# Kernel tuning notes

Measured on AMD Instinct MI355X. Metric: run time of the kernel, lower is better.

## Reference

```python
import jax, jax.numpy as jnp
import numpy as np

T_ITERS = 10
EPS = 1e-5


def setup_inputs() -> dict:
    key = jax.random.key(0)
    B, C, H, W = 64, 256, 56, 56
    X = jax.random.normal(key, (B, C, H, W), dtype=jnp.float32)
    # running_rot buffer: orthogonal rotation per group (g=1)
    M = np.random.default_rng(0).standard_normal((C, C)).astype(np.float32)
    q, _ = np.linalg.qr(M)
    running_rot = jnp.asarray(q[None, :, :])  # [g=1, d, d]
    return {"X": X, "running_rot": running_rot}


def _whiten(X, g, nc):
    # X: [B, C, H, W] -> x: [g, d, m] with m = B*H*W (training-mode IterNorm)
    B, C, H, W = X.shape
    x = jnp.transpose(X, (1, 0, 2, 3)).reshape(g, nc, -1)
    m = x.shape[-1]
    mean = jnp.mean(x, axis=-1, keepdims=True)          # [g, d, 1]
    xc = x - mean                                        # [g, d, m]
    I = jnp.broadcast_to(jnp.eye(nc, dtype=X.dtype), (g, nc, nc))
    Sigma = EPS * I + jnp.matmul(xc, jnp.swapaxes(xc, 1, 2)) * (1.0 / m)
    # rTr = 1 / trace(Sigma) per group
    rTr = 1.0 / jnp.sum(Sigma * I, axis=(1, 2), keepdims=True)  # [g,1,1]
    Sigma_N = Sigma * rTr
    # Newton-Schulz iteration: P_{k+1} = 1.5 P_k - 0.5 P_k^3 Sigma_N
    P = I
    for _ in range(T_ITERS):
        P3 = jnp.matmul(jnp.matmul(P, P), P)
        P = 1.5 * P - 0.5 * jnp.matmul(P3, Sigma_N)
    wm = P * jnp.sqrt(rTr)                               # whitening matrix [g,d,d]
    xn = jnp.matmul(wm, xc)                              # [g, d, m]
    return xn.reshape(C, B, H, W).transpose(1, 0, 2, 3)  # back to [B,C,H,W]


def reference(X, running_rot):
    g, _, nc = running_rot.shape
    B, C, H, W = X.shape
    X_hat = _whiten(X, g, nc)                            # [B, C, H, W]
    Xg = X_hat.reshape(B, g, nc, H, W)
    # rotate whitened features: Q^T alignment, einsum('bgchw,gdc->bgdhw')
    Xr = jnp.einsum('bgchw,gdc->bgdhw', Xg, running_rot)
    return Xr.reshape(B, C, H, W)
```

## Files before the change

### kernel.cpp

```cpp
#include <hip/hip_runtime.h>
#include <math.h>

#define HWn   3136
#define Cn    256
#define KCPB  49
#define NCHUNK 3136
#define INV_M (1.0f/200704.0f)
#define EPSc  1e-5f

typedef __attribute__((ext_vector_type(4))) float f32x4;
typedef __attribute__((ext_vector_type(8))) short s16x8;
typedef __attribute__((ext_vector_type(4))) unsigned short u16x4;

static __device__ __forceinline__ unsigned short f2bf(float f) {
  unsigned int u = __builtin_bit_cast(unsigned int, f);
  u = (u + 0x7fffu + ((u >> 16) & 1u)) >> 16;
  return (unsigned short)u;
}

__global__ __launch_bounds__(1024) void k_gram(const float* __restrict__ X,
                                               float* __restrict__ Gp,
                                               float* __restrict__ Sp,
                                               int nparts) {
  __shared__ __align__(16) unsigned short lds[2][256 * 64];
  const int t = threadIdx.x, p = blockIdx.x;
  const int w = t >> 6, l = t & 63, a = l & 15, g = l >> 4;
  const int swzA = (a & 7) << 3;
  const int crow = t >> 4, sg = t & 15;

  f32x4 acc[16];
#pragma unroll
  for (int j = 0; j < 16; ++j) acc[j] = (f32x4){0.f, 0.f, 0.f, 0.f};
  float sum4[4] = {0.f, 0.f, 0.f, 0.f};
  float vx[16];

  const int start = (int)(((long)NCHUNK * p) / nparts);
  const int end   = (int)(((long)NCHUNK * (p + 1)) / nparts);

#define G_LOADS(CH)                                                           \
  {                                                                           \
    const int b_ = (CH) / KCPB, kc_ = (CH) % KCPB;                            \
    const float* xb_ = X + (long)b_ * Cn * HWn + kc_ * 64;                    \
    _Pragma("unroll")                                                         \
    for (int p4 = 0; p4 < 4; ++p4) {                                          \
      const float4 v = *(const float4*)(xb_ + (long)(p4 * 64 + crow) * HWn + sg * 4); \
      vx[p4 * 4 + 0] = v.x; vx[p4 * 4 + 1] = v.y;                             \
      vx[p4 * 4 + 2] = v.z; vx[p4 * 4 + 3] = v.w;                             \
    }                                                                         \
  }

#define G_CVTWR(BUF)                                                          \
  {                                                                           \
    _Pragma("unroll")                                                         \
    for (int p4 = 0; p4 < 4; ++p4) {                                          \
      const int c_ = p4 * 64 + crow;                                          \
      sum4[p4] += (vx[p4 * 4 + 0] + vx[p4 * 4 + 1])                           \
                + (vx[p4 * 4 + 2] + vx[p4 * 4 + 3]);                          \
      u16x4 h;                                                                \
      h.x = f2bf(vx[p4 * 4 + 0]); h.y = f2bf(vx[p4 * 4 + 1]);                 \
      h.z = f2bf(vx[p4 * 4 + 2]); h.w = f2bf(vx[p4 * 4 + 3]);                 \
      *(u16x4*)(&lds[BUF][0] + ((c_ * 64 + sg * 4) ^ ((c_ & 7) << 3))) = h;   \
    }                                                                         \
  }

  G_LOADS(start);
  G_CVTWR(0);
  __syncthreads();

  for (int ch = start; ch < end; ++ch) {
    const int cur = (ch - start) & 1;
    if (ch + 1 < end) G_LOADS(ch + 1);
    const unsigned short* tile = &lds[cur][0];
#pragma unroll
    for (int kk = 0; kk < 64; kk += 32) {
      const s16x8 fw = *(const s16x8*)(tile + (((w * 16 + a) * 64 + kk + g * 8) ^ swzA));
#pragma unroll
      for (int j = 0; j < 16; ++j) {
        const s16x8 fj = *(const s16x8*)(tile + (((j * 16 + a) * 64 + kk + g * 8) ^ swzA));
        acc[j] = __builtin_amdgcn_mfma_f32_16x16x32_bf16(fw, fj, acc[j], 0, 0, 0);
      }
    }
    if (ch + 1 < end) G_CVTWR(cur ^ 1);
    __syncthreads();
  }
#undef G_LOADS
#undef G_CVTWR

  float* gout = Gp + (long)p * 65536;
#pragma unroll
  for (int j = 0; j < 16; ++j)
#pragma unroll
    for (int r = 0; r < 4; ++r)
      gout[(16 * w + 4 * g + r) * 256 + 16 * j + a] = acc[j][r];

#pragma unroll
  for (int p4 = 0; p4 < 4; ++p4) {
    float s = sum4[p4];
    s += __shfl_xor(s, 1);
    s += __shfl_xor(s, 2);
    s += __shfl_xor(s, 4);
    s += __shfl_xor(s, 8);
    if (a == 0) Sp[(long)p * 256 + p4 * 64 + w * 4 + g] = s;
  }
}

__global__ __launch_bounds__(1024) void k_reduce(const float* __restrict__ Gp,
                                                 const float* __restrict__ Sp,
                                                 float* __restrict__ Sigma,
                                                 float* __restrict__ P0,
                                                 float* __restrict__ diag,
                                                 float* __restrict__ meansum,
                                                 int nparts) {
  __shared__ float red[4][256];
  __shared__ float msh[256];
  const int t = threadIdx.x, c = t & 255, g = t >> 8, j = blockIdx.x;
  const long e = (long)j * 256 + c;
  const int p0 = (nparts * g) >> 2, p1 = (nparts * (g + 1)) >> 2;

  {
    float s = 0.f;
    for (int p = p0; p < p1; ++p) s += Sp[(long)p * 256 + c];
    red[g][c] = s;
  }
  __syncthreads();
  if (g == 0) msh[c] = (red[0][c] + red[1][c]) + (red[2][c] + red[3][c]);
  __syncthreads();

  {
    const float* gp = Gp + (long)p0 * 65536 + e;
    const int np = p1 - p0;
    float s0 = 0.f, s1 = 0.f, s2 = 0.f, s3 = 0.f;
    int p = 0;
#pragma unroll 2
    for (; p + 4 <= np; p += 4) {
      s0 += gp[(long)(p + 0) * 65536];
      s1 += gp[(long)(p + 1) * 65536];
      s2 += gp[(long)(p + 2) * 65536];
      s3 += gp[(long)(p + 3) * 65536];
    }
    for (; p < np; ++p) s0 += gp[(long)p * 65536];
    red[g][c] = (s0 + s1) + (s2 + s3);
  }
  __syncthreads();

  if (g == 0) {
    const float tot = (red[0][c] + red[1][c]) + (red[2][c] + red[3][c]);
    const float mc = msh[c] * INV_M;
    const float mj = msh[j] * INV_M;
    const float sig = tot * INV_M - mj * mc + ((j == c) ? EPSc : 0.f);
    Sigma[e] = sig;
    if (c == j) diag[j] = sig;
    if (j == 0) meansum[c] = msh[c];
  } else if (g == 1) {
    P0[e] = (j == c) ? 1.f : 0.f;
  }
}

__global__ void k_prep(const float* __restrict__ diag, float* __restrict__ scal) {
  __shared__ float r[256];
  const int c = threadIdx.x;
  r[c] = diag[c];
  __syncthreads();
  for (int st = 128; st > 0; st >>= 1) {
    if (c < st) r[c] += r[c + st];
    __syncthreads();
  }
  if (c == 0) {
    const float tr = r[0];
    scal[0] = tr;
    scal[1] = 1.0f / tr;
    scal[2] = sqrtf(1.0f / tr);
  }
}

__global__ __launch_bounds__(1024) void k_ns(const float* __restrict__ Ps,
                                             float* __restrict__ Pd,
                                             const float* __restrict__ Sig,
                                             const float* __restrict__ scal) {
  __shared__ __align__(16) float PT[256][4];
  __shared__ __align__(16) float red[4][256][4];
  const int t = threadIdx.x, c = t & 255, kh = t >> 8, k0 = kh * 64;
  const int r0 = blockIdx.x * 4;

  PT[c][kh] = Ps[(r0 + kh) * 256 + c];
  __syncthreads();

  f32x4 acc;

#define NS_PHASE(BPTR)                                                        \
  {                                                                           \
    acc = (f32x4){0.f, 0.f, 0.f, 0.f};                                        \
    const float* Bb = (BPTR) + (long)k0 * 256 + c;                            \
    _Pragma("unroll 8")                                                       \
    for (int kk = 0; kk < 64; ++kk) {                                         \
      const float b = Bb[(long)kk * 256];                                     \
      const f32x4 a4 = *(const f32x4*)&PT[k0 + kk][0];                        \
      acc += a4 * b;                                                          \
    }                                                                         \
    *(f32x4*)&red[kh][c][0] = acc;                                            \
    __syncthreads();                                                          \
  }

#define NS_COMBINE()                                                          \
  {                                                                           \
    const f32x4 vs = (*(const f32x4*)&red[0][c][0] + *(const f32x4*)&red[1][c][0]) \
                   + (*(const f32x4*)&red[2][c][0] + *(const f32x4*)&red[3][c][0]); \
    if (kh == 0) *(f32x4*)&PT[c][0] = vs;                                     \
    __syncthreads();                                                          \
  }

  NS_PHASE(Ps);
  NS_COMBINE();
  NS_PHASE(Ps);
  NS_COMBINE();
  NS_PHASE(Sig);

  const float rTr = scal[1];
  const float t3 = ((red[0][c][kh] + red[1][c][kh]) + (red[2][c][kh] + red[3][c][kh]));
  const float pr = Ps[(r0 + kh) * 256 + c];
  Pd[(r0 + kh) * 256 + c] = 1.5f * pr - 0.5f * rTr * t3;
#undef NS_PHASE
#undef NS_COMBINE
}

__global__ void k_makeA(const float* __restrict__ rot, const float* __restrict__ P,
                        const float* __restrict__ scal, const float* __restrict__ meansum,
                        unsigned short* __restrict__ Abf, float* __restrict__ bias) {
  __shared__ float Rw[8][256];
  __shared__ float Tw[8][256];
  const int r0 = blockIdx.x * 8, c = threadIdx.x;
#pragma unroll
  for (int r = 0; r < 8; ++r) Rw[r][c] = rot[(r0 + r) * 256 + c];
  __syncthreads();
  float t[8];
#pragma unroll
  for (int r = 0; r < 8; ++r) t[r] = 0.f;
  for (int k = 0; k < 256; ++k) {
    const float pv = P[k * 256 + c];
#pragma unroll
    for (int r = 0; r < 8; ++r) t[r] += Rw[r][k] * pv;
  }
  const float s = scal[2];
  const float mc = meansum[c] * INV_M;
#pragma unroll
  for (int r = 0; r < 8; ++r) {
    const float av = t[r] * s;
    Abf[(r0 + r) * 256 + c] = f2bf(av);
    Tw[r][c] = av * mc;
  }
  __syncthreads();
  for (int st = 128; st > 0; st >>= 1) {
    if (c < st) {
#pragma unroll
      for (int r = 0; r < 8; ++r) Tw[r][c] += Tw[r][c + st];
    }
    __syncthreads();
  }
  if (c == 0) {
#pragma unroll
    for (int r = 0; r < 8; ++r) bias[r0 + r] = Tw[r][0];
  }
}

__global__ __launch_bounds__(1024) void k_apply(const float* __restrict__ X,
                                                const unsigned short* __restrict__ Abf,
                                                const float* __restrict__ bias,
                                                float* __restrict__ out) {
  __shared__ __align__(16) unsigned short lds[2][64 * 256];
  const int t = threadIdx.x, w = t >> 6, l = t & 63, a = l & 15, g = l >> 4;
  const int bid = blockIdx.x;
  const int b = bid >> 3, strip = bid & 7;
  const int ch0 = (49 * strip) >> 3, ch1 = (49 * (strip + 1)) >> 3;

  const int d = 16 * w + a;
  s16x8 af[8];
#pragma unroll
  for (int kk8 = 0; kk8 < 8; ++kk8)
    af[kk8] = *(const s16x8*)(Abf + d * 256 + kk8 * 32 + g * 8);
  const float bd = bias[d];

  const float* xbase = X + (long)b * Cn * HWn;
  float* obase = out + (long)b * Cn * HWn;
  float vx[16];

#define A_LOADS(CH)                                                           \
  {                                                                           \
    const int s0_ = (CH) * 64;                                                \
    _Pragma("unroll")                                                         \
    for (int p4 = 0; p4 < 4; ++p4) {                                          \
      const int c4_ = p4 * 16 + w;                                            \
      const float* xp_ = xbase + (long)(c4_ * 4) * HWn + s0_ + l;             \
      vx[p4 * 4 + 0] = xp_[0];                                                \
      vx[p4 * 4 + 1] = xp_[HWn];                                              \
      vx[p4 * 4 + 2] = xp_[2 * HWn];                                          \
      vx[p4 * 4 + 3] = xp_[3 * HWn];                                          \
    }                                                                         \
  }

#define A_CVTWR(BUF)                                                          \
  {                                                                           \
    _Pragma("unroll")                                                         \
    for (int p4 = 0; p4 < 4; ++p4) {                                          \
      const int c4_ = p4 * 16 + w;                                            \
      u16x4 h;                                                                \
      h.x = f2bf(vx[p4 * 4 + 0]); h.y = f2bf(vx[p4 * 4 + 1]);                 \
      h.z = f2bf(vx[p4 * 4 + 2]); h.w = f2bf(vx[p4 * 4 + 3]);                 \
      *(u16x4*)(&lds[BUF][0] + ((l * 256 + c4_ * 4) ^ ((l & 7) << 3))) = h;   \
    }                                                                         \
  }

  A_LOADS(ch0);
  A_CVTWR(0);
  __syncthreads();

  for (int ch = ch0; ch < ch1; ++ch) {
    const int cur = (ch - ch0) & 1;
    if (ch + 1 < ch1) A_LOADS(ch + 1);

    const unsigned short* tile = &lds[cur][0];
    f32x4 acc[4];
#pragma unroll
    for (int st = 0; st < 4; ++st) acc[st] = (f32x4){0.f, 0.f, 0.f, 0.f};
#pragma unroll
    for (int kk8 = 0; kk8 < 8; ++kk8) {
#pragma unroll
      for (int st = 0; st < 4; ++st) {
        const s16x8 xf = *(const s16x8*)(tile + (((st * 16 + a) * 256 + kk8 * 32 + g * 8) ^ ((a & 7) << 3)));
        acc[st] = __builtin_amdgcn_mfma_f32_16x16x32_bf16(xf, af[kk8], acc[st], 0, 0, 0);
      }
    }
    const int s0 = ch * 64;
#pragma unroll
    for (int st = 0; st < 4; ++st) {
      const f32x4 o = acc[st] - bd;
      *(f32x4*)(obase + (long)d * HWn + s0 + st * 16 + 4 * g) = o;
    }

    if (ch + 1 < ch1) A_CVTWR(cur ^ 1);
    __syncthreads();
  }
#undef A_LOADS
#undef A_CVTWR
}

extern "C" void kernel_launch(void* const* d_in, const int* in_sizes, int n_in,
                              void* d_out, int out_size, void* d_ws, size_t ws_size,
                              hipStream_t stream) {
  const float* X = (const float*)d_in[0];
  const float* rot = (const float*)d_in[1];
  float* out = (float*)d_out;

  auto need = [](int np) -> size_t {
    return (size_t)4 * ((size_t)np * 65536 + (size_t)np * 256 + 3 * 65536
                        + 256 + 256 + 16 + 256)
         + (size_t)2 * 65536;
  };
  int nparts = 256;
  while (nparts > 4 && need(nparts) > ws_size) nparts >>= 1;

  float* w = (float*)d_ws;
  float* Gp = w;       w += (size_t)nparts * 65536;
  float* Sp = w;       w += (size_t)nparts * 256;
  float* Sigma = w;    w += 65536;
  float* P0 = w;       w += 65536;
  float* P1 = w;       w += 65536;
  float* diag = w;     w += 256;
  float* meansum = w;  w += 256;
  float* scal = w;     w += 16;
  float* bias = w;     w += 256;
  unsigned short* Abf = (unsigned short*)w;

  k_gram<<<dim3(nparts), dim3(1024), 0, stream>>>(X, Gp, Sp, nparts);
  k_reduce<<<dim3(256), dim3(1024), 0, stream>>>(Gp, Sp, Sigma, P0, diag, meansum, nparts);
  k_prep<<<dim3(1), dim3(256), 0, stream>>>(diag, scal);
  float* ps = P0;
  float* pd = P1;
  for (int i = 0; i < 10; ++i) {
    k_ns<<<dim3(64), dim3(1024), 0, stream>>>(ps, pd, Sigma, scal);
    float* tmp = ps; ps = pd; pd = tmp;
  }
  k_makeA<<<dim3(32), dim3(256), 0, stream>>>(rot, ps, scal, meansum, Abf, bias);
  k_apply<<<dim3(512), dim3(1024), 0, stream>>>(X, Abf, bias, out);
}
```

Measured before the change: 312.9 us.

## Fuse Newton-Schulz iterations and makeA into one persistent kernel with grid barrier

Replaces the prep kernel, ten separate Newton-Schulz launches and the makeA kernel with a single persistent 64-block kernel. It computes the trace locally, peels the first iteration analytically (P1 = 1.5I - 0.5 rTr Sigma), and synchronises blocks between iterations with an atomic spin barrier. The intent is to remove about eleven kernel launch gaps from this serial chain. It also vectorises the Gram partial reduction with float4 loads across 16 slices and uses nontemporal stores for the output. The spin barrier relies on all 64 blocks being co-resident, and the barrier counter is reset in the preceding kernel.

```diff
diff --git a/kernel.cpp b/kernel.cpp
--- a/kernel.cpp
+++ b/kernel.cpp
@@ -16,6 +16,18 @@
   unsigned int u = __builtin_bit_cast(unsigned int, f);
   u = (u + 0x7fffu + ((u >> 16) & 1u)) >> 16;
   return (unsigned short)u;
+}
+
+static __device__ __forceinline__ void grid_sync(unsigned int* bar, unsigned int target) {
+  __syncthreads();
+  if (threadIdx.x == 0) {
+    __threadfence();
+    atomicAdd(bar, 1u);
+    while (__hip_atomic_load(bar, __ATOMIC_RELAXED, __HIP_MEMORY_SCOPE_AGENT) < target)
+      __builtin_amdgcn_s_sleep(2);
+  }
+  __syncthreads();
+  __threadfence();
 }
 
 __global__ __launch_bounds__(1024) void k_gram(const float* __restrict__ X,
@@ -107,83 +119,83 @@
 __global__ __launch_bounds__(1024) void k_reduce(const float* __restrict__ Gp,
                                                  const float* __restrict__ Sp,
                                                  float* __restrict__ Sigma,
-                                                 float* __restrict__ P0,
                                                  float* __restrict__ diag,
                                                  float* __restrict__ meansum,
+                                                 unsigned int* __restrict__ bar,
                                                  int nparts) {
-  __shared__ float red[4][256];
+  __shared__ float redA[4][256];
   __shared__ float msh[256];
-  const int t = threadIdx.x, c = t & 255, g = t >> 8, j = blockIdx.x;
-  const long e = (long)j * 256 + c;
-  const int p0 = (nparts * g) >> 2, p1 = (nparts * (g + 1)) >> 2;
+  __shared__ __align__(16) float redB[16][256];
+  const int t = threadIdx.x, j = blockIdx.x;
+  const int c = t & 255, g = t >> 8;
 
   {
     float s = 0.f;
-    for (int p = p0; p < p1; ++p) s += Sp[(long)p * 256 + c];
-    red[g][c] = s;
-  }
-  __syncthreads();
-  if (g == 0) msh[c] = (red[0][c] + red[1][c]) + (red[2][c] + red[3][c]);
-  __syncthreads();
+    const int pa0 = (nparts * g) >> 2, pa1 = (nparts * (g + 1)) >> 2;
+    for (int p = pa0; p < pa1; ++p) s += Sp[(long)p * 256 + c];
+    redA[g][c] = s;
+  }
+  __syncthreads();
+  if (g == 0) msh[c] = (redA[0][c] + redA[1][c]) + (redA[2][c] + redA[3][c]);
 
   {
-    const float* gp = Gp + (long)p0 * 65536 + e;
-    const int np = p1 - p0;
-    float s0 = 0.f, s1 = 0.f, s2 = 0.f, s3 = 0.f;
-    int p = 0;
-#pragma unroll 2
-    for (; p + 4 <= np; p += 4) {
-      s0 += gp[(long)(p + 0) * 65536];
-      s1 += gp[(long)(p + 1) * 65536];
-      s2 += gp[(long)(p + 2) * 65536];
-      s3 += gp[(long)(p + 3) * 65536];
-    }
-    for (; p < np; ++p) s0 += gp[(long)p * 65536];
-    red[g][c] = (s0 + s1) + (s2 + s3);
-  }
-  __syncthreads();
-
-  if (g == 0) {
-    const float tot = (red[0][c] + red[1][c]) + (red[2][c] + red[3][c]);
-    const float mc = msh[c] * INV_M;
+    const int c4 = (t & 63) * 4, sl = t >> 6;
+    const int pb0 = (nparts * sl) >> 4, pb1 = (nparts * (sl + 1)) >> 4;
+    const float* gp = Gp + (long)pb0 * 65536 + (long)j * 256 + c4;
+    f32x4 s4 = (f32x4){0.f, 0.f, 0.f, 0.f};
+    for (int p = pb0; p < pb1; ++p) { s4 += *(const f32x4*)gp; gp += 65536; }
+    *(f32x4*)&redB[sl][c4] = s4;
+  }
+  __syncthreads();
+
+  if (t < 256) {
+    float t0 = 0.f, t1 = 0.f;
+#pragma unroll
+    for (int sl = 0; sl < 16; sl += 2) { t0 += redB[sl][t]; t1 += redB[sl + 1][t]; }
+    const float tot = t0 + t1;
+    const float mc = msh[t] * INV_M;
     const float mj = msh[j] * INV_M;
-    const float sig = tot * INV_M - mj * mc + ((j == c) ? EPSc : 0.f);
-    Sigma[e] = sig;
-    if (c == j) diag[j] = sig;
-    if (j == 0) meansum[c] = msh[c];
-  } else if (g == 1) {
-    P0[e] = (j == c) ? 1.f : 0.f;
-  }
-}
-
-__global__ void k_prep(const float* __restrict__ diag, float* __restrict__ scal) {
-  __shared__ float r[256];
-  const int c = threadIdx.x;
-  r[c] = diag[c];
-  __syncthreads();
-  for (int st = 128; st > 0; st >>= 1) {
-    if (c < st) r[c] += r[c + st];
-    __syncthreads();
-  }
-  if (c == 0) {
-    const float tr = r[0];
-    scal[0] = tr;
-    scal[1] = 1.0f / tr;
-    scal[2] = sqrtf(1.0f / tr);
-  }
-}
-
-__global__ __launch_bounds__(1024) void k_ns(const float* __restrict__ Ps,
-                                             float* __restrict__ Pd,
-                                             const float* __restrict__ Sig,
-                                             const float* __restrict__ scal) {
+    const float sig = tot * INV_M - mj * mc + ((j == t) ? EPSc : 0.f);
+    Sigma[(long)j * 256 + t] = sig;
+    if (t == j) diag[j] = sig;
+    if (j == 0) {
+      meansum[t] = msh[t];
+      if (t == 0)
+        __hip_atomic_store(bar, 0u, __ATOMIC_RELAXED, __HIP_MEMORY_SCOPE_SYSTEM);
+    }
+  }
+}
+
+__global__ __launch_bounds__(1024) void k_ns_fused(const float* __restrict__ Sig,
+                                                   float* __restrict__ P0,
+                                                   float* __restrict__ P1,
+                                                   const float* __restrict__ diag,
+                                                   const float* __restrict__ rot,
+                                                   const float* __restrict__ meansum,
+                                                   unsigned int* __restrict__ bar,
+                                                   unsigned short* __restrict__ Abf,
+                                                   float* __restrict__ bias) {
   __shared__ __align__(16) float PT[256][4];
   __shared__ __align__(16) float red[4][256][4];
+  __shared__ float trs[256];
   const int t = threadIdx.x, c = t & 255, kh = t >> 8, k0 = kh * 64;
   const int r0 = blockIdx.x * 4;
 
-  PT[c][kh] = Ps[(r0 + kh) * 256 + c];
-  __syncthreads();
+  if (t < 256) trs[t] = diag[t];
+  __syncthreads();
+  for (int st = 128; st > 0; st >>= 1) {
+    if (t < st) trs[t] += trs[t + st];
+    __syncthreads();
+  }
+  const float rTr = 1.0f / trs[0];
+
+  {
+    const int row = r0 + kh;
+    const float sv = Sig[(long)row * 256 + c];
+    P1[(long)row * 256 + c] = ((row == c) ? 1.5f : 0.f) - 0.5f * rTr * sv;
+  }
+  unsigned int tgt = 64;
+  grid_sync(bar, tgt); tgt += 64;
 
   f32x4 acc;
 
@@ -209,56 +221,64 @@
     __syncthreads();                                                          \
   }
 
-  NS_PHASE(Ps);
-  NS_COMBINE();
-  NS_PHASE(Ps);
-  NS_COMBINE();
-  NS_PHASE(Sig);
-
-  const float rTr = scal[1];
-  const float t3 = ((red[0][c][kh] + red[1][c][kh]) + (red[2][c][kh] + red[3][c][kh]));
-  const float pr = Ps[(r0 + kh) * 256 + c];
-  Pd[(r0 + kh) * 256 + c] = 1.5f * pr - 0.5f * rTr * t3;
+  for (int it = 1; it < 10; ++it) {
+    const float* Ps = (it & 1) ? P1 : P0;
+    float* Pd = (it & 1) ? P0 : P1;
+
+    PT[c][kh] = Ps[(long)(r0 + kh) * 256 + c];
+    __syncthreads();
+
+    NS_PHASE(Ps);
+    NS_COMBINE();
+    NS_PHASE(Ps);
+    NS_COMBINE();
+    NS_PHASE(Sig);
+
+    const float t3 = ((red[0][c][kh] + red[1][c][kh]) + (red[2][c][kh] + red[3][c][kh]));
+    const float pr = Ps[(long)(r0 + kh) * 256 + c];
+    Pd[(long)(r0 + kh) * 256 + c] = 1.5f * pr - 0.5f * rTr * t3;
+
+    grid_sync(bar, tgt); tgt += 64;
+  }
 #undef NS_PHASE
 #undef NS_COMBINE
-}
-
-__global__ void k_makeA(const float* __restrict__ rot, const float* __restrict__ P,
-                        const float* __restrict__ scal, const float* __restrict__ meansum,
-                        unsigned short* __restrict__ Abf, float* __restrict__ bias) {
-  __shared__ float Rw[8][256];
-  __shared__ float Tw[8][256];
-  const int r0 = blockIdx.x * 8, c = threadIdx.x;
-#pragma unroll
-  for (int r = 0; r < 8; ++r) Rw[r][c] = rot[(r0 + r) * 256 + c];
-  __syncthreads();
-  float t[8];
-#pragma unroll
-  for (int r = 0; r < 8; ++r) t[r] = 0.f;
-  for (int k = 0; k < 256; ++k) {
-    const float pv = P[k * 256 + c];
-#pragma unroll
-    for (int r = 0; r < 8; ++r) t[r] += Rw[r][k] * pv;
-  }
-  const float s = scal[2];
-  const float mc = meansum[c] * INV_M;
-#pragma unroll
-  for (int r = 0; r < 8; ++r) {
-    const float av = t[r] * s;
-    Abf[(r0 + r) * 256 + c] = f2bf(av);
-    Tw[r][c] = av * mc;
+
+  PT[c][kh] = rot[(long)(r0 + kh) * 256 + c];
+  __syncthreads();
+  {
+    acc = (f32x4){0.f, 0.f, 0.f, 0.f};
+    const float* Bb = P0 + (long)k0 * 256 + c;
+#pragma unroll 8
+    for (int kk = 0; kk < 64; ++kk) {
+      const float b = Bb[(long)kk * 256];
+      const f32x4 a4 = *(const f32x4*)&PT[k0 + kk][0];
+      acc += a4 * b;
+    }
+    *(f32x4*)&red[kh][c][0] = acc;
+  }
+  __syncthreads();
+  const float s2 = sqrtf(rTr);
+  if (t < 256) {
+    f32x4 av = (*(const f32x4*)&red[0][t][0] + *(const f32x4*)&red[1][t][0])
+             + (*(const f32x4*)&red[2][t][0] + *(const f32x4*)&red[3][t][0]);
+    av *= s2;
+#pragma unroll
+    for (int i = 0; i < 4; ++i) Abf[(r0 + i) * 256 + t] = f2bf(av[i]);
+    const float mc = meansum[t] * INV_M;
+    *(f32x4*)&PT[t][0] = av * mc;
   }
   __syncthreads();
   for (int st = 128; st > 0; st >>= 1) {
-    if (c < st) {
-#pragma unroll
-      for (int r = 0; r < 8; ++r) Tw[r][c] += Tw[r][c + st];
-    }
-    __syncthreads();
-  }
-  if (c == 0) {
-#pragma unroll
-    for (int r = 0; r < 8; ++r) bias[r0 + r] = Tw[r][0];
+    if (t < st) {
+      const f32x4 v = *(const f32x4*)&PT[t][0] + *(const f32x4*)&PT[t + st][0];
+      *(f32x4*)&PT[t][0] = v;
+    }
+    __syncthreads();
+  }
+  if (t == 0) {
+    const f32x4 bv = *(const f32x4*)&PT[0][0];
+#pragma unroll
+    for (int i = 0; i < 4; ++i) bias[r0 + i] = bv[i];
   }
 }
 
@@ -333,7 +353,7 @@
 #pragma unroll
     for (int st = 0; st < 4; ++st) {
       const f32x4 o = acc[st] - bd;
-      *(f32x4*)(obase + (long)d * HWn + s0 + st * 16 + 4 * g) = o;
+      __builtin_nontemporal_store(o, (f32x4*)(obase + (long)d * HWn + s0 + st * 16 + 4 * g));
     }
 
     if (ch + 1 < ch1) A_CVTWR(cur ^ 1);
@@ -352,7 +372,7 @@
 
   auto need = [](int np) -> size_t {
     return (size_t)4 * ((size_t)np * 65536 + (size_t)np * 256 + 3 * 65536
-                        + 256 + 256 + 16 + 256)
+                        + 256 + 256 + 256 + 16)
          + (size_t)2 * 65536;
   };
   int nparts = 256;
@@ -366,19 +386,12 @@
   float* P1 = w;       w += 65536;
   float* diag = w;     w += 256;
   float* meansum = w;  w += 256;
-  float* scal = w;     w += 16;
   float* bias = w;     w += 256;
+  unsigned int* bar = (unsigned int*)w;  w += 16;
   unsigned short* Abf = (unsigned short*)w;
 
   k_gram<<<dim3(nparts), dim3(1024), 0, stream>>>(X, Gp, Sp, nparts);
-  k_reduce<<<dim3(256), dim3(1024), 0, stream>>>(Gp, Sp, Sigma, P0, diag, meansum, nparts);
-  k_prep<<<dim3(1), dim3(256), 0, stream>>>(diag, scal);
-  float* ps = P0;
-  float* pd = P1;
-  for (int i = 0; i < 10; ++i) {
-    k_ns<<<dim3(64), dim3(1024), 0, stream>>>(ps, pd, Sigma, scal);
-    float* tmp = ps; ps = pd; pd = tmp;
-  }
-  k_makeA<<<dim3(32), dim3(256), 0, stream>>>(rot, ps, scal, meansum, Abf, bias);
+  k_reduce<<<dim3(256), dim3(1024), 0, stream>>>(Gp, Sp, Sigma, diag, meansum, bar, nparts);
+  k_ns_fused<<<dim3(64), dim3(1024), 0, stream>>>(Sigma, P0, P1, diag, rot, meansum, bar, Abf, bias);
   k_apply<<<dim3(512), dim3(1024), 0, stream>>>(X, Abf, bias, out);
 }
```

New measurement: 482.4 us. 54.2% more time.
